# Kernel optimization log

Measured on AMD Instinct MI355X. Metric: run time of the kernel, lower is better.

Reference implementation:

```python
import jax, jax.numpy as jnp
import numpy as np
from jax import lax


def lstm_cell(x, h, c, Wih, Whh, bih, bhh):
    # PyTorch LSTMCell gate order: i, f, g, o
    gates = x @ Wih.T + h @ Whh.T + bih + bhh  # (B, 4H)
    i, f, g, o = jnp.split(gates, 4, axis=-1)
    c_new = jax.nn.sigmoid(f) * c + jax.nn.sigmoid(i) * jnp.tanh(g)
    h_new = jax.nn.sigmoid(o) * jnp.tanh(c_new)
    return h_new, c_new


def setup_inputs() -> dict:
    key = jax.random.key(0)
    ks = jax.random.split(key, 9)
    B, T = 1024, 4096
    I, H, O = 1, 20, 1  # input_size, hidden_size, output_size
    return {
        "input_data": jax.random.normal(ks[0], (B, T), dtype=jnp.float32),
        # weights ~ N(0, 0.1) as in the torch module; biases small uniform-ish
        "W_ih1": 0.1 * jax.random.normal(ks[1], (4 * H, I), dtype=jnp.float32),
        "W_hh1": 0.1 * jax.random.normal(ks[2], (4 * H, H), dtype=jnp.float32),
        "b_ih1": 0.05 * jax.random.normal(ks[3], (4 * H,), dtype=jnp.float32),
        "b_hh1": 0.05 * jax.random.normal(ks[4], (4 * H,), dtype=jnp.float32),
        "W_ih2": 0.1 * jax.random.normal(ks[5], (4 * O, H), dtype=jnp.float32),
        "W_hh2": 0.1 * jax.random.normal(ks[6], (4 * O, O), dtype=jnp.float32),
        "b_ih2": 0.05 * jax.random.normal(ks[7], (4 * O,), dtype=jnp.float32),
        "b_hh2": 0.05 * jax.random.normal(ks[8], (4 * O,), dtype=jnp.float32),
        "future": 16,
    }


def reference(input_data, W_ih1, W_hh1, b_ih1, b_hh1,
              W_ih2, W_hh2, b_ih2, b_hh2, future):
    B = input_data.shape[0]
    H = W_hh1.shape[1]
    O = W_hh2.shape[1]
    dt = input_data.dtype
    h1 = jnp.zeros((B, H), dt)
    c1 = jnp.zeros((B, H), dt)
    h2 = jnp.zeros((B, O), dt)
    c2 = jnp.zeros((B, O), dt)

    xs = input_data.T[:, :, None]  # (T, B, 1)

    def step(carry, x_t):
        h1, c1, h2, c2 = carry
        h1, c1 = lstm_cell(x_t, h1, c1, W_ih1, W_hh1, b_ih1, b_hh1)
        h2, c2 = lstm_cell(c1, h2, c2, W_ih2, W_hh2, b_ih2, b_hh2)
        return (h1, c1, h2, c2), c2  # emit c_t2, as in the torch code

    carry, outs = lax.scan(step, (h1, c1, h2, c2), xs)  # outs: (T, B, O)

    def fstep(carry, _):
        h1, c1, h2, c2 = carry
        h1, c1 = lstm_cell(c2, h1, c1, W_ih1, W_hh1, b_ih1, b_hh1)
        h2, c2 = lstm_cell(c1, h2, c2, W_ih2, W_hh2, b_ih2, b_hh2)
        return (h1, c1, h2, c2), c2

    _, fouts = lax.scan(fstep, carry, None, length=future)  # (F, B, O)

    all_out = jnp.concatenate([outs, fouts], axis=0)  # (T+F, B, 1)
    # torch: stack(dim=1).squeeze(2) -> (B, T+F)
    return all_out[..., 0].T
```

## Files before the change

### kernel.cpp

```cpp
#include <hip/hip_runtime.h>

typedef float v2f __attribute__((ext_vector_type(2)));

template <int C>
__device__ __forceinline__ float qperm(float x) {
    return __int_as_float(__builtin_amdgcn_mov_dpp(__float_as_int(x), C, 0xF, 0xF, false));
}
__device__ __forceinline__ float rl(float x, int l) {
    return __int_as_float(__builtin_amdgcn_readlane(__float_as_int(x), l));
}
__device__ __forceinline__ float rcp_(float x) { return __builtin_amdgcn_rcpf(x); }
__device__ __forceinline__ float ex2(float x)  { return __builtin_amdgcn_exp2f(x); }

__device__ __forceinline__ float act2(float a, float m) {
    float r = rcp_(1.0f + ex2(-a));
    return fmaf(m, r - 1.0f, 1.0f);
}
__device__ __forceinline__ float tanh2(float x) {
    return fmaf(2.0f, rcp_(1.0f + ex2(-2.885390082f * x)) - 1.0f, 1.0f);
}

#define FMA2(a, b, c) __builtin_elementwise_fma(a, b, c)

#define DOTP(P, R) { \
    v2f z0 = P##0 * s0; v2f z1 = P##1 * s1; \
    z0 = FMA2(P##2, s2, z0); z1 = FMA2(P##3, s3, z1); \
    z0 = FMA2(P##4, s4, z0); z1 = FMA2(P##5, s5, z1); \
    z0 = FMA2(P##6, s6, z0); z1 = FMA2(P##7, s7, z1); \
    z0 = FMA2(P##8, s8, z0); z1 = FMA2(P##9, s9, z1); \
    z0 = z0 + z1; R += z0.x + z0.y; }

#define LOADQ(BASE) \
    float4 A4 = (BASE)[0], B4 = (BASE)[1], C4 = (BASE)[2], D4 = (BASE)[3], E4 = (BASE)[4]; \
    v2f s0 = {A4.x, A4.y}, s1 = {A4.z, A4.w}, s2 = {B4.x, B4.y}, s3 = {B4.z, B4.w}, \
        s4 = {C4.x, C4.y}, s5 = {C4.z, C4.w}, s6 = {D4.x, D4.y}, s7 = {D4.z, D4.w}, \
        s8 = {E4.x, E4.y}, s9 = {E4.z, E4.w};

#define L2COMBINE(DEST_IDX_EXPR) { \
    float i2 = qperm<0x00>(actL), f2 = qperm<0x55>(actL); \
    float g2 = qperm<0xAA>(actL), o2 = qperm<0xFF>(actL); \
    float c2n = fmaf(f2, c2my, i2 * g2); \
    h2my = o2 * tanh2(c2n); \
    c2my = c2n; \
    if (lane == 40) op[DEST_IDX_EXPR] = c2n; }

__global__ __launch_bounds__(64, 1)
void lstm2_kernel(const float* __restrict__ x_in,
                  const float* __restrict__ Wih1,
                  const float* __restrict__ Whh1,
                  const float* __restrict__ bih1,
                  const float* __restrict__ bhh1,
                  const float* __restrict__ Wih2,
                  const float* __restrict__ Whh2,
                  const float* __restrict__ bih2,
                  const float* __restrict__ bhh2,
                  float* __restrict__ out,
                  int T, int F)
{
    const int  lane = threadIdx.x;
    const int  b    = blockIdx.x;
    const int  p    = lane & 1;
    int        j    = lane >> 1; if (j > 19) j = 19;
    const bool isL2 = (lane >= 40 && lane < 44);
    const int  g    = isL2 ? (lane - 40) : 0;

    __shared__ float sb[48];
    if (lane < 48) sb[lane] = 0.0f;
    __builtin_amdgcn_wave_barrier();

    const int rA = j + 20 * p;
    const int rB = 40 + j + 20 * p;

    const float* WArow = isL2 ? (Wih2 + g * 20) : (Whh1 + rA * 20);
    const float* WBrow = Whh1 + rB * 20;

    const float4* wap = (const float4*)WArow;
    const float4* wbp = (const float4*)WBrow;
    float4 La0 = wap[0], La1 = wap[1], La2 = wap[2], La3 = wap[3], La4 = wap[4];
    float4 Lb0 = wbp[0], Lb1 = wbp[1], Lb2 = wbp[2], Lb3 = wbp[3], Lb4 = wbp[4];
    v2f wa0 = {La0.x,La0.y}, wa1 = {La0.z,La0.w}, wa2 = {La1.x,La1.y}, wa3 = {La1.z,La1.w},
        wa4 = {La2.x,La2.y}, wa5 = {La2.z,La2.w}, wa6 = {La3.x,La3.y}, wa7 = {La3.z,La3.w},
        wa8 = {La4.x,La4.y}, wa9 = {La4.z,La4.w};
    v2f wb0 = {Lb0.x,Lb0.y}, wb1 = {Lb0.z,Lb0.w}, wb2 = {Lb1.x,Lb1.y}, wb3 = {Lb1.z,Lb1.w},
        wb4 = {Lb2.x,Lb2.y}, wb5 = {Lb2.z,Lb2.w}, wb6 = {Lb3.x,Lb3.y}, wb7 = {Lb3.z,Lb3.w},
        wb8 = {Lb4.x,Lb4.y}, wb9 = {Lb4.z,Lb4.w};

    float wxA, wxB, bsA, bsB;
    {
        float u_wxA = Wih1[rA], u_wxB = Wih1[rB];
        float u_bsA = bih1[rA] + bhh1[rA];
        float u_bsB = bih1[rB] + bhh1[rB];
        float l_wxA = Whh2[g];
        float l_bsA = bih2[g] + bhh2[g];
        wxA = isL2 ? l_wxA : u_wxA;
        bsA = isL2 ? l_bsA : u_bsA;
        wxB = u_wxB;  bsB = u_bsB;
    }

    const float mB = p ? 1.0f : 2.0f;
    const float mL = (lane == 42) ? 2.0f : 1.0f;
    const float mA = isL2 ? mL : 1.0f;

    const float LOG2E = 1.4426950408889634f;
    const float kA = LOG2E * mA;
    const float kB = LOG2E * mB;
    {
        v2f kA2 = {kA, kA}, kB2 = {kB, kB};
        wa0 *= kA2; wa1 *= kA2; wa2 *= kA2; wa3 *= kA2; wa4 *= kA2;
        wa5 *= kA2; wa6 *= kA2; wa7 *= kA2; wa8 *= kA2; wa9 *= kA2;
        wb0 *= kB2; wb1 *= kB2; wb2 *= kB2; wb3 *= kB2; wb4 *= kB2;
        wb5 *= kB2; wb6 *= kB2; wb7 *= kB2; wb8 *= kB2; wb9 *= kB2;
        wxA *= kA; bsA *= kA; wxB *= kB; bsB *= kB;
    }

    const float4* sp  = (const float4*)(sb + (isL2 ? 24 : 0));
    const float4* spc = (const float4*)(sb + 24);
    const float4* sph = (const float4*)sb;

    float c1my = 0.0f, c2my = 0.0f, h2my = 0.0f;

    const float* xp = x_in + (long)b * T;
    float*       op = out  + (long)b * (T + F);

    float xr = xp[0];
    float x1 = xp[T > 1 ? 1 : 0];
    float x2 = xp[T > 2 ? 2 : 0];

    for (int t = 0; t < T; ++t) {
        LOADQ(sp)
        int tn = t + 3; tn = (tn < T) ? tn : (T - 1);
        const float xf = xp[tn];

        const float xinA = isL2 ? h2my : xr;
        float aA = fmaf(wxA, xinA, bsA);
        float aB = fmaf(wxB, xr,   bsB);
        DOTP(wa, aA)
        DOTP(wb, aB)

        float actA = act2(aA, mA);
        float actB = act2(aB, mB);

        float nbA = qperm<0xB1>(actA);
        float nbB = qperm<0xB1>(actB);
        float gi = p ? nbA : actA;
        float gf = p ? actA : nbA;
        float gg = p ? nbB : actB;
        float go = p ? actB : nbB;

        float cn = fmaf(gf, c1my, gi * gg);
        c1my = cn;
        float hn = go * tanh2(cn);
        if (!p && lane < 40) { sb[24 + j] = cn; sb[j] = hn; }

        float actL = actA;
        if (t > 0) L2COMBINE(t - 1)

        asm volatile("" ::: "memory");
        __builtin_amdgcn_wave_barrier();
        xr = x1; x1 = x2; x2 = xf;
    }

    {
        LOADQ(spc)
        float aL = fmaf(wxA, h2my, bsA);
        DOTP(wa, aL)
        float actL = act2(aL, mA);
        L2COMBINE(T - 1)
    }
    float xF = rl(c2my, 40);

    for (int i = 0; i < F; ++i) {
        {
            LOADQ(sph)
            float aA = fmaf(wxA, xF, bsA);
            float aB = fmaf(wxB, xF, bsB);
            DOTP(wa, aA)
            DOTP(wb, aB)
            float actA = act2(aA, mA);
            float actB = act2(aB, mB);
            float nbA = qperm<0xB1>(actA);
            float nbB = qperm<0xB1>(actB);
            float gi = p ? nbA : actA;
            float gf = p ? actA : nbA;
            float gg = p ? nbB : actB;
            float go = p ? actB : nbB;
            float cn = fmaf(gf, c1my, gi * gg);
            c1my = cn;
            float hn = go * tanh2(cn);
            if (!p && lane < 40) { sb[24 + j] = cn; sb[j] = hn; }
        }
        asm volatile("" ::: "memory");
        __builtin_amdgcn_wave_barrier();
        {
            LOADQ(spc)
            float aL = fmaf(wxA, h2my, bsA);
            DOTP(wa, aL)
            float actL = act2(aL, mA);
            L2COMBINE(T + i)
        }
        xF = rl(c2my, 40);
        asm volatile("" ::: "memory");
        __builtin_amdgcn_wave_barrier();
    }
}

extern "C" void kernel_launch(void* const* d_in, const int* in_sizes, int n_in,
                              void* d_out, int out_size, void* d_ws, size_t ws_size,
                              hipStream_t stream) {
    const float* x    = (const float*)d_in[0];
    const float* Wih1 = (const float*)d_in[1];
    const float* Whh1 = (const float*)d_in[2];
    const float* bih1 = (const float*)d_in[3];
    const float* bhh1 = (const float*)d_in[4];
    const float* Wih2 = (const float*)d_in[5];
    const float* Whh2 = (const float*)d_in[6];
    const float* bih2 = (const float*)d_in[7];
    const float* bhh2 = (const float*)d_in[8];
    float* out = (float*)d_out;

    const int B = 1024;
    const int T = in_sizes[0] / B;
    const int F = out_size / B - T;

    hipLaunchKernelGGL(lstm2_kernel, dim3(B), dim3(64), 0, stream,
                       x, Wih1, Whh1, bih1, bhh1, Wih2, Whh2, bih2, bhh2, out, T, F);
}
```

Baseline: 1.225 ms.

## Unroll LSTM time loop by four, batch output stores, shorten dependency chains

The main recurrence is unrolled by four time steps. The layer-2 combine now runs at the start of each step, where it can overlap with the layer-1 dot products, and the four emitted c2 values go out as one float4 store instead of four scalar stores. The dot product uses four partial accumulators instead of two to shorten the serial FMA chain. The sigmoid and tanh epilogues are folded into fewer FMAs. The unrolled loop assumes T is a multiple of four and that the output rows are 16-byte aligned.

```diff
diff --git a/kernel.cpp b/kernel.cpp
--- a/kernel.cpp
+++ b/kernel.cpp
@@ -12,23 +12,16 @@
 __device__ __forceinline__ float rcp_(float x) { return __builtin_amdgcn_rcpf(x); }
 __device__ __forceinline__ float ex2(float x)  { return __builtin_amdgcn_exp2f(x); }
 
-__device__ __forceinline__ float act2(float a, float m) {
-    float r = rcp_(1.0f + ex2(-a));
-    return fmaf(m, r - 1.0f, 1.0f);
-}
-__device__ __forceinline__ float tanh2(float x) {
-    return fmaf(2.0f, rcp_(1.0f + ex2(-2.885390082f * x)) - 1.0f, 1.0f);
-}
-
 #define FMA2(a, b, c) __builtin_elementwise_fma(a, b, c)
+#define NTANH_K 2.885390082f
 
 #define DOTP(P, R) { \
-    v2f z0 = P##0 * s0; v2f z1 = P##1 * s1; \
-    z0 = FMA2(P##2, s2, z0); z1 = FMA2(P##3, s3, z1); \
+    v2f z0 = P##0 * s0, z1 = P##1 * s1, z2 = P##2 * s2, z3 = P##3 * s3; \
     z0 = FMA2(P##4, s4, z0); z1 = FMA2(P##5, s5, z1); \
-    z0 = FMA2(P##6, s6, z0); z1 = FMA2(P##7, s7, z1); \
+    z2 = FMA2(P##6, s6, z2); z3 = FMA2(P##7, s7, z3); \
     z0 = FMA2(P##8, s8, z0); z1 = FMA2(P##9, s9, z1); \
-    z0 = z0 + z1; R += z0.x + z0.y; }
+    z0 = z0 + z1; z2 = z2 + z3; z0 = z0 + z2; \
+    R += z0.x + z0.y; }
 
 #define LOADQ(BASE) \
     float4 A4 = (BASE)[0], B4 = (BASE)[1], C4 = (BASE)[2], D4 = (BASE)[3], E4 = (BASE)[4]; \
@@ -36,13 +29,43 @@
         s4 = {C4.x, C4.y}, s5 = {C4.z, C4.w}, s6 = {D4.x, D4.y}, s7 = {D4.z, D4.w}, \
         s8 = {E4.x, E4.y}, s9 = {E4.z, E4.w};
 
-#define L2COMBINE(DEST_IDX_EXPR) { \
+#define L2C(RB) { \
     float i2 = qperm<0x00>(actL), f2 = qperm<0x55>(actL); \
     float g2 = qperm<0xAA>(actL), o2 = qperm<0xFF>(actL); \
     float c2n = fmaf(f2, c2my, i2 * g2); \
-    h2my = o2 * tanh2(c2n); \
+    float rt2 = rcp_(1.0f + ex2(-NTANH_K * c2n)); \
+    h2my = fmaf(o2 + o2, rt2, -o2); \
     c2my = c2n; \
-    if (lane == 40) op[DEST_IDX_EXPR] = c2n; }
+    RB = c2n; }
+
+#define STEP(TT, POS, XUSE, XFVAR, ...) { \
+    LOADQ(sp) \
+    int tn_ = (TT) + (POS) + 3; tn_ = tn_ < T ? tn_ : T - 1; \
+    XFVAR = xp[tn_]; \
+    __VA_ARGS__ \
+    const float xinA = isL2 ? h2my : (XUSE); \
+    float aA = fmaf(wxA, xinA, bsA); \
+    float aB = fmaf(wxB, (XUSE), bsB); \
+    DOTP(wa, aA) \
+    DOTP(wb, aB) \
+    float rA_ = rcp_(1.0f + ex2(-aA)); \
+    float rB_ = rcp_(1.0f + ex2(-aB)); \
+    float actA = fmaf(mA, rA_, onemA); \
+    float actB = fmaf(mB, rB_, onemB); \
+    float nbA = qperm<0xB1>(actA); \
+    float nbB = qperm<0xB1>(actB); \
+    float gi = p ? nbA : actA; \
+    float gf = p ? actA : nbA; \
+    float gg = p ? nbB : actB; \
+    float go = p ? actB : nbB; \
+    float cn = fmaf(gf, c1my, gi * gg); \
+    c1my = cn; \
+    float rT_ = rcp_(1.0f + ex2(-NTANH_K * cn)); \
+    float hn = fmaf(go + go, rT_, -go); \
+    if (!p && lane < 40) { sb[24 + j] = cn; sb[j] = hn; } \
+    actL = actA; \
+    asm volatile("" ::: "memory"); \
+}
 
 __global__ __launch_bounds__(64, 1)
 void lstm2_kernel(const float* __restrict__ x_in,
@@ -67,6 +90,7 @@
     __shared__ float sb[48];
     if (lane < 48) sb[lane] = 0.0f;
     __builtin_amdgcn_wave_barrier();
+    asm volatile("" ::: "memory");
 
     const int rA = j + 20 * p;
     const int rB = 40 + j + 20 * p;
@@ -100,6 +124,7 @@
     const float mB = p ? 1.0f : 2.0f;
     const float mL = (lane == 42) ? 2.0f : 1.0f;
     const float mA = isL2 ? mL : 1.0f;
+    const float onemA = 1.0f - mA, onemB = 1.0f - mB;
 
     const float LOG2E = 1.4426950408889634f;
     const float kA = LOG2E * mA;
@@ -118,55 +143,38 @@
     const float4* sph = (const float4*)sb;
 
     float c1my = 0.0f, c2my = 0.0f, h2my = 0.0f;
+    float actL = 0.0f;
+    float rb0 = 0.0f, rb1 = 0.0f, rb2 = 0.0f, rb3 = 0.0f;
 
     const float* xp = x_in + (long)b * T;
     float*       op = out  + (long)b * (T + F);
 
-    float xr = xp[0];
-    float x1 = xp[T > 1 ? 1 : 0];
-    float x2 = xp[T > 2 ? 2 : 0];
-
-    for (int t = 0; t < T; ++t) {
-        LOADQ(sp)
-        int tn = t + 3; tn = (tn < T) ? tn : (T - 1);
-        const float xf = xp[tn];
-
-        const float xinA = isL2 ? h2my : xr;
-        float aA = fmaf(wxA, xinA, bsA);
-        float aB = fmaf(wxB, xr,   bsB);
-        DOTP(wa, aA)
-        DOTP(wb, aB)
-
-        float actA = act2(aA, mA);
-        float actB = act2(aB, mB);
-
-        float nbA = qperm<0xB1>(actA);
-        float nbB = qperm<0xB1>(actB);
-        float gi = p ? nbA : actA;
-        float gf = p ? actA : nbA;
-        float gg = p ? nbB : actB;
-        float go = p ? actB : nbB;
-
-        float cn = fmaf(gf, c1my, gi * gg);
-        c1my = cn;
-        float hn = go * tanh2(cn);
-        if (!p && lane < 40) { sb[24 + j] = cn; sb[j] = hn; }
-
-        float actL = actA;
-        if (t > 0) L2COMBINE(t - 1)
-
-        asm volatile("" ::: "memory");
-        __builtin_amdgcn_wave_barrier();
-        xr = x1; x1 = x2; x2 = xf;
-    }
-
+    float xA = xp[0];
+    float xB = xp[T > 1 ? 1 : 0];
+    float xC = xp[T > 2 ? 2 : 0];
+
+    for (int t = 0; t < T; t += 4) {
+        float nx0, nx1, nx2, nx3;
+        STEP(t, 0, xA, nx0, if (t > 0) { L2C(rb2) })
+        STEP(t, 1, xB, nx1, if (t > 0) { L2C(rb3)
+            if (lane == 40) { float4 v4; v4.x = rb0; v4.y = rb1; v4.z = rb2; v4.w = rb3;
+                              *(float4*)(op + t - 4) = v4; } })
+        STEP(t, 2, xC, nx2, L2C(rb0))
+        STEP(t, 3, nx0, nx3, L2C(rb1))
+        xA = nx1; xB = nx2; xC = nx3;
+    }
+
+    L2C(rb2)
     {
         LOADQ(spc)
         float aL = fmaf(wxA, h2my, bsA);
         DOTP(wa, aL)
-        float actL = act2(aL, mA);
-        L2COMBINE(T - 1)
-    }
+        float rL_ = rcp_(1.0f + ex2(-aL));
+        actL = fmaf(mA, rL_, onemA);
+    }
+    L2C(rb3)
+    if (lane == 40) { float4 v4; v4.x = rb0; v4.y = rb1; v4.z = rb2; v4.w = rb3;
+                      *(float4*)(op + T - 4) = v4; }
     float xF = rl(c2my, 40);
 
     for (int i = 0; i < F; ++i) {
@@ -176,8 +184,10 @@
             float aB = fmaf(wxB, xF, bsB);
             DOTP(wa, aA)
             DOTP(wb, aB)
-            float actA = act2(aA, mA);
-            float actB = act2(aB, mB);
+            float rA_ = rcp_(1.0f + ex2(-aA));
+            float rB_ = rcp_(1.0f + ex2(-aB));
+            float actA = fmaf(mA, rA_, onemA);
+            float actB = fmaf(mB, rB_, onemB);
             float nbA = qperm<0xB1>(actA);
             float nbB = qperm<0xB1>(actB);
             float gi = p ? nbA : actA;
@@ -186,7 +196,8 @@
             float go = p ? actB : nbB;
             float cn = fmaf(gf, c1my, gi * gg);
             c1my = cn;
-            float hn = go * tanh2(cn);
+            float rT_ = rcp_(1.0f + ex2(-NTANH_K * cn));
+            float hn = fmaf(go + go, rT_, -go);
             if (!p && lane < 40) { sb[24 + j] = cn; sb[j] = hn; }
         }
         asm volatile("" ::: "memory");
@@ -195,8 +206,11 @@
             LOADQ(spc)
             float aL = fmaf(wxA, h2my, bsA);
             DOTP(wa, aL)
-            float actL = act2(aL, mA);
-            L2COMBINE(T + i)
+            float rL_ = rcp_(1.0f + ex2(-aL));
+            actL = fmaf(mA, rL_, onemA);
+            float dummy;
+            L2C(dummy)
+            if (lane == 40) op[T + i] = dummy;
         }
         xF = rl(c2my, 40);
         asm volatile("" ::: "memory");
```

New measurement: 987.8 us. -19.4%, faster.
